# Kernel optimization log

Hardware: AMD Instinct MI355X
Metric: run time of the kernel (lower is better)

## Reference

```python
import jax, jax.numpy as jnp
import numpy as np

N_NODES = 20000


def gcn_layer(x, W, b, src, dst, n):
    # linear transform first (as in PyG GCNConv)
    h = x @ W  # [N, out]
    # add self-loops
    loop = jnp.arange(n, dtype=src.dtype)
    src_f = jnp.concatenate([src, loop])
    dst_f = jnp.concatenate([dst, loop])
    # symmetric degree normalization: deg computed on destination (col) index
    ones = jnp.ones_like(dst_f, dtype=h.dtype)
    deg = jax.ops.segment_sum(ones, dst_f, num_segments=n)
    dinv = jnp.where(deg > 0, jax.lax.rsqrt(deg), 0.0)
    norm = dinv[src_f] * dinv[dst_f]  # [E+N]
    # gather-normalize-scatter aggregation
    msgs = h[src_f] * norm[:, None]  # [E+N, out]
    out = jax.ops.segment_sum(msgs, dst_f, num_segments=n)
    return out + b


def setup_inputs() -> dict:
    key = jax.random.key(0)
    k = jax.random.split(key, 6)
    x = jax.random.normal(k[0], (N_NODES, 256), dtype=jnp.float32)
    edge_index = jax.random.randint(k[1], (2, 320000), 0, N_NODES, dtype=jnp.int64)
    s1 = 1.0 / np.sqrt(256)
    s2 = 1.0 / np.sqrt(1600)
    W1 = jax.random.uniform(k[2], (256, 1600), jnp.float32, -s1, s1)
    b1 = jnp.zeros((1600,), jnp.float32)
    W2 = jax.random.uniform(k[3], (1600, 400), jnp.float32, -s2, s2)
    b2 = jnp.zeros((400,), jnp.float32)
    return {"x": x, "edge_index": edge_index, "W1": W1, "b1": b1, "W2": W2, "b2": b2}


def reference(x, edge_index, W1, b1, W2, b2):
    src, dst = edge_index[0], edge_index[1]
    n = x.shape[0]
    h = jax.nn.relu(gcn_layer(x, W1, b1, src, dst, n))
    return gcn_layer(h, W2, b2, src, dst, n)
```

## Files before the change

### kernel.cpp

```cpp
#include <hip/hip_runtime.h>
#include <hip/hip_bf16.h>
#include <stdint.h>

typedef _Float16 f16;
typedef _Float16 f16x8 __attribute__((ext_vector_type(8)));
typedef _Float16 f16v4 __attribute__((ext_vector_type(4)));
typedef float f32x4 __attribute__((ext_vector_type(4)));

__device__ __forceinline__ void gload_lds16(const f16* g, f16* l) {
  __builtin_amdgcn_global_load_lds(
      (const __attribute__((address_space(1))) void*)g,
      (__attribute__((address_space(3))) void*)l, 16, 0, 0);
}

__device__ __forceinline__ int edge_at(const void* ep, int isI64, long long idx) {
  if (isI64) return (int)((const long long*)ep)[idx];
  return ((const int*)ep)[idx];
}

__global__ void detect_kernel(const unsigned int* __restrict__ e, int* __restrict__ flag) {
  __shared__ int any;
  if (threadIdx.x == 0) any = 0;
  __syncthreads();
  for (int idx = 1 + 2 * (int)threadIdx.x; idx < 4096; idx += 512) {
    if (e[idx] != 0u) any = 1;
  }
  __syncthreads();
  if (threadIdx.x == 0) flag[0] = any ? 0 : 1;
}

__global__ void deg_kernel(const void* __restrict__ ep, const int* __restrict__ flag,
                           int* __restrict__ indeg, int E) {
  int e = blockIdx.x * blockDim.x + threadIdx.x;
  if (e >= E) return;
  int i64 = flag[0];
  int d = edge_at(ep, i64, (long long)E + e);
  atomicAdd(&indeg[d], 1);
}

__global__ void dinv_kernel(const int* __restrict__ indeg, float* __restrict__ dinv, int n) {
  int i = blockIdx.x * blockDim.x + threadIdx.x;
  if (i < n) dinv[i] = rsqrtf((float)(indeg[i] + 1));
}

__global__ __launch_bounds__(1024) void prefix_kernel(const int* __restrict__ indeg,
                                                      int* __restrict__ rowptr, int n) {
  __shared__ int wsum[16];
  int t = threadIdx.x;
  int lane = t & 63;
  int w = t >> 6;
  int carry = 0;
  if (t == 0) rowptr[0] = 0;
  for (int base = 0; base < n; base += 1024) {
    int i = base + t;
    int v = (i < n) ? indeg[i] : 0;
    int sv = v;
#pragma unroll
    for (int off = 1; off < 64; off <<= 1) {
      int u = __shfl_up(sv, off, 64);
      if (lane >= off) sv += u;
    }
    if (lane == 63) wsum[w] = sv;
    __syncthreads();
    if (w == 0 && lane < 16) {
      int ws = wsum[lane];
#pragma unroll
      for (int off = 1; off < 16; off <<= 1) {
        int u = __shfl_up(ws, off, 64);
        if (lane >= off) ws += u;
      }
      wsum[lane] = ws;
    }
    __syncthreads();
    int woff = (w > 0) ? wsum[w - 1] : 0;
    if (i < n) rowptr[i + 1] = carry + woff + sv;
    carry += wsum[15];
    __syncthreads();
  }
}

__global__ void scatter_kernel(const void* __restrict__ ep, const int* __restrict__ flag,
                               const int* __restrict__ rowptr, int* __restrict__ cursor,
                               int* __restrict__ colsrc, int E) {
  int e = blockIdx.x * blockDim.x + threadIdx.x;
  if (e >= E) return;
  int i64 = flag[0];
  int s = edge_at(ep, i64, (long long)e);
  int d = edge_at(ep, i64, (long long)E + e);
  int pos = atomicAdd(&cursor[d], 1);
  colsrc[rowptr[d] + pos] = s;
}

__global__ __launch_bounds__(256) void agg1_kernel(const float* __restrict__ x,
                                                   const float* __restrict__ dinv,
                                                   const int* __restrict__ rowptr,
                                                   const int* __restrict__ colsrc,
                                                   f16* __restrict__ xa, int n) {
  int wave = threadIdx.x >> 6;
  int lane = threadIdx.x & 63;
  int i = blockIdx.x * 4 + wave;
  if (i >= n) return;
  const float4* xp = (const float4*)x;
  float di = dinv[i];
  float4 s = xp[(size_t)i * 64 + lane];
  float ax = di * s.x, ay = di * s.y, az = di * s.z, aw = di * s.w;
  float bx = 0.f, by = 0.f, bz = 0.f, bw = 0.f;
  int beg = rowptr[i], end = rowptr[i + 1];
  int j = beg;
  for (; j + 3 < end; j += 4) {
    int s0 = colsrc[j], s1 = colsrc[j + 1], s2 = colsrc[j + 2], s3 = colsrc[j + 3];
    float w0 = dinv[s0], w1 = dinv[s1], w2 = dinv[s2], w3 = dinv[s3];
    float4 v0 = xp[(size_t)s0 * 64 + lane];
    float4 v1 = xp[(size_t)s1 * 64 + lane];
    float4 v2 = xp[(size_t)s2 * 64 + lane];
    float4 v3 = xp[(size_t)s3 * 64 + lane];
    ax += w0 * v0.x + w2 * v2.x; ay += w0 * v0.y + w2 * v2.y;
    az += w0 * v0.z + w2 * v2.z; aw += w0 * v0.w + w2 * v2.w;
    bx += w1 * v1.x + w3 * v3.x; by += w1 * v1.y + w3 * v3.y;
    bz += w1 * v1.z + w3 * v3.z; bw += w1 * v1.w + w3 * v3.w;
  }
  for (; j < end; ++j) {
    int s0 = colsrc[j];
    float w0 = dinv[s0];
    float4 v0 = xp[(size_t)s0 * 64 + lane];
    ax += w0 * v0.x; ay += w0 * v0.y; az += w0 * v0.z; aw += w0 * v0.w;
  }
  f16v4 r;
  r[0] = (f16)(di * (ax + bx));
  r[1] = (f16)(di * (ay + by));
  r[2] = (f16)(di * (az + bz));
  r[3] = (f16)(di * (aw + bw));
  *(f16v4*)&xa[(size_t)i * 256 + lane * 4] = r;
}

__global__ __launch_bounds__(256) void agg2_kernel(const f16* __restrict__ g,
                                                   const float* __restrict__ dinv,
                                                   const int* __restrict__ rowptr,
                                                   const int* __restrict__ colsrc,
                                                   const float* __restrict__ bias,
                                                   float* __restrict__ out, int n, int F) {
  int wave = threadIdx.x >> 6;
  int lane = threadIdx.x & 63;
  int i = blockIdx.x * 4 + wave;
  if (i >= n) return;
  int base = lane * 8;
  if (base >= F) return;
  float di = dinv[i];
  f16x8 sv = *(const f16x8*)&g[(size_t)i * F + base];
  float a[8], b[8];
#pragma unroll
  for (int r = 0; r < 8; ++r) { a[r] = di * (float)sv[r]; b[r] = 0.f; }
  int beg = rowptr[i], end = rowptr[i + 1];
  int j = beg;
  for (; j + 1 < end; j += 2) {
    int s0 = colsrc[j], s1 = colsrc[j + 1];
    float w0 = dinv[s0], w1 = dinv[s1];
    f16x8 v0 = *(const f16x8*)&g[(size_t)s0 * F + base];
    f16x8 v1 = *(const f16x8*)&g[(size_t)s1 * F + base];
#pragma unroll
    for (int r = 0; r < 8; ++r) { a[r] += w0 * (float)v0[r]; b[r] += w1 * (float)v1[r]; }
  }
  if (j < end) {
    int s0 = colsrc[j];
    float w0 = dinv[s0];
    f16x8 v0 = *(const f16x8*)&g[(size_t)s0 * F + base];
#pragma unroll
    for (int r = 0; r < 8; ++r) a[r] += w0 * (float)v0[r];
  }
  float4 o0, o1;
  float4 bv0 = *(const float4*)&bias[base];
  float4 bv1 = *(const float4*)&bias[base + 4];
  o0.x = di * (a[0] + b[0]) + bv0.x; o0.y = di * (a[1] + b[1]) + bv0.y;
  o0.z = di * (a[2] + b[2]) + bv0.z; o0.w = di * (a[3] + b[3]) + bv0.w;
  o1.x = di * (a[4] + b[4]) + bv1.x; o1.y = di * (a[5] + b[5]) + bv1.y;
  o1.z = di * (a[6] + b[6]) + bv1.z; o1.w = di * (a[7] + b[7]) + bv1.w;
  *(float4*)&out[(size_t)i * F + base] = o0;
  *(float4*)&out[(size_t)i * F + base + 4] = o1;
}

__global__ void castT_kernel(const float* __restrict__ W, f16* __restrict__ Wt, int K, int N) {
  int idx = blockIdx.x * 256 + threadIdx.x;
  if (idx >= K * N) return;
  int k = idx / N;
  int nn = idx - k * N;
  Wt[(size_t)nn * K + k] = (f16)W[idx];
}

__global__ __launch_bounds__(256) void gemm1_f16(
    const f16* __restrict__ A, const f16* __restrict__ B,
    const float* __restrict__ bias, f16* __restrict__ C,
    int M, int N, int K) {
  __shared__ __align__(16) f16 smem[2 * 128 * 64];
  f16* sA = smem;
  f16* sB = smem + 128 * 64;
  const int m0 = blockIdx.y * 128;
  const int n0 = blockIdx.x * 128;
  const int lane = threadIdx.x & 63;
  const int wave = threadIdx.x >> 6;
  const int wm = (wave & 1) * 64;
  const int wn = (wave >> 1) * 64;
  const int lrow = lane & 15;
  const int quad = lane >> 4;

  f32x4 acc[4][4];
#pragma unroll
  for (int i = 0; i < 4; ++i)
#pragma unroll
    for (int j = 0; j < 4; ++j) acc[i][j] = (f32x4)(0.f);

  for (int k0 = 0; k0 < K; k0 += 64) {
#pragma unroll
    for (int i = 0; i < 4; ++i) {
      int ch = (i * 4 + wave) * 64 + lane;
      int r = ch >> 3;
      int cg = (ch & 7) ^ (r & 7);
      int gr = min(m0 + r, M - 1);
      gload_lds16(&A[(size_t)gr * K + k0 + cg * 8], &sA[(size_t)(i * 4 + wave) * 512]);
      int gn = min(n0 + r, N - 1);
      gload_lds16(&B[(size_t)gn * K + k0 + cg * 8], &sB[(size_t)(i * 4 + wave) * 512]);
    }
    __syncthreads();
#pragma unroll
    for (int kk = 0; kk < 2; ++kk) {
      f16x8 af[4], bf[4];
      int cg = quad + kk * 4;
#pragma unroll
      for (int i = 0; i < 4; ++i) {
        int ra = wm + i * 16 + lrow;
        af[i] = *(const f16x8*)&sA[ra * 64 + ((cg ^ (ra & 7)) * 8)];
        int rb = wn + i * 16 + lrow;
        bf[i] = *(const f16x8*)&sB[rb * 64 + ((cg ^ (rb & 7)) * 8)];
      }
#pragma unroll
      for (int i = 0; i < 4; ++i)
#pragma unroll
        for (int j = 0; j < 4; ++j)
          acc[i][j] = __builtin_amdgcn_mfma_f32_16x16x32_f16(af[i], bf[j], acc[i][j], 0, 0, 0);
    }
    __syncthreads();
  }

  const int crow = quad * 4;
  const int ccol = lane & 15;
#pragma unroll
  for (int j = 0; j < 4; ++j) {
    int col = wn + j * 16 + ccol;
    int gcol = n0 + col;
    float bv = (gcol < N) ? bias[gcol] : 0.f;
#pragma unroll
    for (int i = 0; i < 4; ++i) {
#pragma unroll
      for (int r = 0; r < 4; ++r) {
        int row = wm + i * 16 + crow + r;
        smem[row * 128 + col] = (f16)fmaxf(acc[i][j][r] + bv, 0.f);
      }
    }
  }
  __syncthreads();
#pragma unroll
  for (int i = 0; i < 8; ++i) {
    int ch = i * 256 + (int)threadIdx.x;
    int r = ch >> 4;
    int cc = ch & 15;
    int grow = m0 + r;
    int gcol = n0 + cc * 8;
    if (grow < M && gcol < N)
      *(uint4*)&C[(size_t)grow * N + gcol] = *(const uint4*)&smem[r * 128 + cc * 8];
  }
}

__global__ __launch_bounds__(256) void gemm2_f16(
    const f16* __restrict__ A, const f16* __restrict__ B, f16* __restrict__ C,
    int M, int N, int K) {
  __shared__ __align__(16) f16 smem[128 * 64 + 80 * 64];
  f16* sA = smem;
  f16* sB = smem + 128 * 64;

  const int mtc = (M + 127) >> 7;
  const int ntc = (N + 79) / 80;
  const int fullm = mtc & ~7;
  const int full = fullm * ntc;
  int idf = blockIdx.x;
  int mt, nt;
  if (idf < full) {
    int gsz = 8 * ntc;
    int grp = idf / gsz;
    int r = idf - grp * gsz;
    mt = grp * 8 + (r & 7);
    nt = r >> 3;
  } else {
    int r = idf - full;
    int rem = mtc - fullm;
    mt = fullm + r % rem;
    nt = r / rem;
  }
  const int m0 = mt * 128;
  const int n0 = nt * 80;
  const int lane = threadIdx.x & 63;
  const int wave = threadIdx.x >> 6;
  const int wm = wave * 32;
  const int lrow = lane & 15;
  const int quad = lane >> 4;

  f32x4 acc[2][5];
#pragma unroll
  for (int i = 0; i < 2; ++i)
#pragma unroll
    for (int j = 0; j < 5; ++j) acc[i][j] = (f32x4)(0.f);

  for (int k0 = 0; k0 < K; k0 += 64) {
#pragma unroll
    for (int i = 0; i < 4; ++i) {
      int ch = (i * 4 + wave) * 64 + lane;
      int r = ch >> 3;
      int cg = (ch & 7) ^ (r & 7);
      int gr = min(m0 + r, M - 1);
      gload_lds16(&A[(size_t)gr * K + k0 + cg * 8], &sA[(size_t)(i * 4 + wave) * 512]);
    }
#pragma unroll
    for (int i = 0; i < 3; ++i) {
      if (i * 4 + wave < 10) {
        int ch = (i * 4 + wave) * 64 + lane;
        int r = ch >> 3;
        int cg = (ch & 7) ^ (r & 7);
        gload_lds16(&B[(size_t)(n0 + r) * K + k0 + cg * 8], &sB[(size_t)(i * 4 + wave) * 512]);
      }
    }
    __syncthreads();
#pragma unroll
    for (int kk = 0; kk < 2; ++kk) {
      f16x8 af[2], bf[5];
      int cg = quad + kk * 4;
#pragma unroll
      for (int i = 0; i < 2; ++i) {
        int ra = wm + i * 16 + lrow;
        af[i] = *(const f16x8*)&sA[ra * 64 + ((cg ^ (ra & 7)) * 8)];
      }
#pragma unroll
      for (int j = 0; j < 5; ++j) {
        int rb = j * 16 + lrow;
        bf[j] = *(const f16x8*)&sB[rb * 64 + ((cg ^ (rb & 7)) * 8)];
      }
#pragma unroll
      for (int i = 0; i < 2; ++i)
#pragma unroll
        for (int j = 0; j < 5; ++j)
          acc[i][j] = __builtin_amdgcn_mfma_f32_16x16x32_f16(af[i], bf[j], acc[i][j], 0, 0, 0);
    }
    __syncthreads();
  }

  const int crow = quad * 4;
  const int ccol = lane & 15;
#pragma unroll
  for (int j = 0; j < 5; ++j) {
    int col = j * 16 + ccol;
#pragma unroll
    for (int i = 0; i < 2; ++i) {
#pragma unroll
      for (int r = 0; r < 4; ++r) {
        int row = wm + i * 16 + crow + r;
        smem[row * 80 + col] = (f16)acc[i][j][r];
      }
    }
  }
  __syncthreads();
#pragma unroll
  for (int i = 0; i < 5; ++i) {
    int ch = i * 256 + (int)threadIdx.x;
    int r = ch / 10;
    int rem = ch - 10 * r;
    int grow = m0 + r;
    if (grow < M)
      *(uint4*)&C[(size_t)grow * N + n0 + rem * 8] = *(const uint4*)&smem[r * 80 + rem * 8];
  }
}

extern "C" void kernel_launch(void* const* d_in, const int* in_sizes, int n_in,
                              void* d_out, int out_size, void* d_ws, size_t ws_size,
                              hipStream_t stream) {
  const float* x = (const float*)d_in[0];
  const void* edges = d_in[1];
  const float* W1 = (const float*)d_in[2];
  const float* b1 = (const float*)d_in[3];
  const float* W2 = (const float*)d_in[4];
  const float* b2 = (const float*)d_in[5];
  float* out = (float*)d_out;

  const int N1 = in_sizes[3];
  const int N2 = in_sizes[5];
  const int K1 = in_sizes[2] / N1;
  const int K2 = in_sizes[4] / N2;
  const int n = in_sizes[0] / K1;
  const int E = in_sizes[1] / 2;

  char* ws = (char*)d_ws;
  size_t o = 0;
  auto take = [&](size_t bytes) {
    char* p = ws + o;
    o += (bytes + 255) & ~(size_t)255;
    return p;
  };
  int* indeg = (int*)take((size_t)n * 4);
  int* cursor = (int*)take((size_t)n * 4);
  int* flag = (int*)take(4);
  size_t zero_bytes = o;
  int* rowptr = (int*)take((size_t)(n + 1) * 4);
  int* colsrc = (int*)take((size_t)E * 4);
  float* dinv = (float*)take((size_t)n * 4);
  f16* xa = (f16*)take((size_t)n * K1 * 2);
  f16* w1t = (f16*)take((size_t)K1 * N1 * 2);
  f16* w2t = (f16*)take((size_t)K2 * N2 * 2);
  f16* h = (f16*)take((size_t)n * N1 * 2);
  f16* g = (f16*)take((size_t)n * N2 * 2);

  hipMemsetAsync(d_ws, 0, zero_bytes, stream);

  detect_kernel<<<1, 256, 0, stream>>>((const unsigned int*)edges, flag);
  deg_kernel<<<(E + 255) / 256, 256, 0, stream>>>(edges, flag, indeg, E);
  dinv_kernel<<<(n + 255) / 256, 256, 0, stream>>>(indeg, dinv, n);
  prefix_kernel<<<1, 1024, 0, stream>>>(indeg, rowptr, n);
  scatter_kernel<<<(E + 255) / 256, 256, 0, stream>>>(edges, flag, rowptr, cursor, colsrc, E);

  castT_kernel<<<(K1 * N1 + 255) / 256, 256, 0, stream>>>(W1, w1t, K1, N1);
  castT_kernel<<<(K2 * N2 + 255) / 256, 256, 0, stream>>>(W2, w2t, K2, N2);

  agg1_kernel<<<(n + 3) / 4, 256, 0, stream>>>(x, dinv, rowptr, colsrc, xa, n);
  {
    dim3 grid((N1 + 127) / 128, (n + 127) / 128);
    gemm1_f16<<<grid, 256, 0, stream>>>(xa, w1t, b1, h, n, N1, K1);
  }
  {
    int mtc = (n + 127) / 128;
    int ntc = (N2 + 79) / 80;
    gemm2_f16<<<mtc * ntc, 256, 0, stream>>>(h, w2t, g, n, N2, K2);
  }
  agg2_kernel<<<(n + 3) / 4, 256, 0, stream>>>(g, dinv, rowptr, colsrc, b2, out, n, N2);
}
```

Baseline: 302.5 us.

## Pre-scale features by source dinv and drop per-edge dinv gathers

Folds the source-side degree normalization into the features before aggregation. Layer 1 now runs an xcast kernel that writes x*dinv as fp16, and gemm2 scales its output rows by dinv, so both aggregation loops skip the per-edge dinv gather and multiply. The change also merges the dinv computation into the prefix kernel, merges the two weight-cast launches, and widens the agg2 unroll to four edges. Gather traffic in agg1 is halved by reading fp16 instead of fp32, at the cost of an extra cast pass and buffer plus earlier fp16 rounding of the scaled inputs.

```diff
diff --git a/kernel.cpp b/kernel.cpp
--- a/kernel.cpp
+++ b/kernel.cpp
@@ -38,13 +38,9 @@
   atomicAdd(&indeg[d], 1);
 }
 
-__global__ void dinv_kernel(const int* __restrict__ indeg, float* __restrict__ dinv, int n) {
-  int i = blockIdx.x * blockDim.x + threadIdx.x;
-  if (i < n) dinv[i] = rsqrtf((float)(indeg[i] + 1));
-}
-
 __global__ __launch_bounds__(1024) void prefix_kernel(const int* __restrict__ indeg,
-                                                      int* __restrict__ rowptr, int n) {
+                                                      int* __restrict__ rowptr,
+                                                      float* __restrict__ dinv, int n) {
   __shared__ int wsum[16];
   int t = threadIdx.x;
   int lane = t & 63;
@@ -54,6 +50,7 @@
   for (int base = 0; base < n; base += 1024) {
     int i = base + t;
     int v = (i < n) ? indeg[i] : 0;
+    if (i < n) dinv[i] = rsqrtf((float)(v + 1));
     int sv = v;
 #pragma unroll
     for (int off = 1; off < 64; off <<= 1) {
@@ -91,7 +88,22 @@
   colsrc[rowptr[d] + pos] = s;
 }
 
-__global__ __launch_bounds__(256) void agg1_kernel(const float* __restrict__ x,
+__global__ void xcast_kernel(const float* __restrict__ x, const float* __restrict__ dinv,
+                             f16* __restrict__ xs, int n) {
+  int c = blockIdx.x * 256 + threadIdx.x;
+  if (c >= n * 64) return;
+  int row = c >> 6;
+  float d = dinv[row];
+  float4 v = ((const float4*)x)[c];
+  f16v4 r;
+  r[0] = (f16)(d * v.x);
+  r[1] = (f16)(d * v.y);
+  r[2] = (f16)(d * v.z);
+  r[3] = (f16)(d * v.w);
+  ((f16v4*)xs)[c] = r;
+}
+
+__global__ __launch_bounds__(256) void agg1_kernel(const f16* __restrict__ xs,
                                                    const float* __restrict__ dinv,
                                                    const int* __restrict__ rowptr,
                                                    const int* __restrict__ colsrc,
@@ -100,40 +112,38 @@
   int lane = threadIdx.x & 63;
   int i = blockIdx.x * 4 + wave;
   if (i >= n) return;
-  const float4* xp = (const float4*)x;
+  const f16v4* xp = (const f16v4*)xs;
   float di = dinv[i];
-  float4 s = xp[(size_t)i * 64 + lane];
-  float ax = di * s.x, ay = di * s.y, az = di * s.z, aw = di * s.w;
-  float bx = 0.f, by = 0.f, bz = 0.f, bw = 0.f;
+  f16v4 s = xp[(size_t)i * 64 + lane];
+  float a0 = (float)s[0], a1 = (float)s[1], a2 = (float)s[2], a3 = (float)s[3];
+  float b0 = 0.f, b1 = 0.f, b2 = 0.f, b3 = 0.f;
   int beg = rowptr[i], end = rowptr[i + 1];
   int j = beg;
   for (; j + 3 < end; j += 4) {
     int s0 = colsrc[j], s1 = colsrc[j + 1], s2 = colsrc[j + 2], s3 = colsrc[j + 3];
-    float w0 = dinv[s0], w1 = dinv[s1], w2 = dinv[s2], w3 = dinv[s3];
-    float4 v0 = xp[(size_t)s0 * 64 + lane];
-    float4 v1 = xp[(size_t)s1 * 64 + lane];
-    float4 v2 = xp[(size_t)s2 * 64 + lane];
-    float4 v3 = xp[(size_t)s3 * 64 + lane];
-    ax += w0 * v0.x + w2 * v2.x; ay += w0 * v0.y + w2 * v2.y;
-    az += w0 * v0.z + w2 * v2.z; aw += w0 * v0.w + w2 * v2.w;
-    bx += w1 * v1.x + w3 * v3.x; by += w1 * v1.y + w3 * v3.y;
-    bz += w1 * v1.z + w3 * v3.z; bw += w1 * v1.w + w3 * v3.w;
+    f16v4 v0 = xp[(size_t)s0 * 64 + lane];
+    f16v4 v1 = xp[(size_t)s1 * 64 + lane];
+    f16v4 v2 = xp[(size_t)s2 * 64 + lane];
+    f16v4 v3 = xp[(size_t)s3 * 64 + lane];
+    a0 += (float)v0[0] + (float)v2[0]; a1 += (float)v0[1] + (float)v2[1];
+    a2 += (float)v0[2] + (float)v2[2]; a3 += (float)v0[3] + (float)v2[3];
+    b0 += (float)v1[0] + (float)v3[0]; b1 += (float)v1[1] + (float)v3[1];
+    b2 += (float)v1[2] + (float)v3[2]; b3 += (float)v1[3] + (float)v3[3];
   }
   for (; j < end; ++j) {
     int s0 = colsrc[j];
-    float w0 = dinv[s0];
-    float4 v0 = xp[(size_t)s0 * 64 + lane];
-    ax += w0 * v0.x; ay += w0 * v0.y; az += w0 * v0.z; aw += w0 * v0.w;
+    f16v4 v0 = xp[(size_t)s0 * 64 + lane];
+    a0 += (float)v0[0]; a1 += (float)v0[1]; a2 += (float)v0[2]; a3 += (float)v0[3];
   }
   f16v4 r;
-  r[0] = (f16)(di * (ax + bx));
-  r[1] = (f16)(di * (ay + by));
-  r[2] = (f16)(di * (az + bz));
-  r[3] = (f16)(di * (aw + bw));
+  r[0] = (f16)(di * (a0 + b0));
+  r[1] = (f16)(di * (a1 + b1));
+  r[2] = (f16)(di * (a2 + b2));
+  r[3] = (f16)(di * (a3 + b3));
   *(f16v4*)&xa[(size_t)i * 256 + lane * 4] = r;
 }
 
-__global__ __launch_bounds__(256) void agg2_kernel(const f16* __restrict__ g,
+__global__ __launch_bounds__(256) void agg2_kernel(const f16* __restrict__ gs,
                                                    const float* __restrict__ dinv,
                                                    const int* __restrict__ rowptr,
                                                    const int* __restrict__ colsrc,
@@ -146,26 +156,29 @@
   int base = lane * 8;
   if (base >= F) return;
   float di = dinv[i];
-  f16x8 sv = *(const f16x8*)&g[(size_t)i * F + base];
+  f16x8 sv = *(const f16x8*)&gs[(size_t)i * F + base];
   float a[8], b[8];
 #pragma unroll
-  for (int r = 0; r < 8; ++r) { a[r] = di * (float)sv[r]; b[r] = 0.f; }
+  for (int r = 0; r < 8; ++r) { a[r] = (float)sv[r]; b[r] = 0.f; }
   int beg = rowptr[i], end = rowptr[i + 1];
   int j = beg;
-  for (; j + 1 < end; j += 2) {
-    int s0 = colsrc[j], s1 = colsrc[j + 1];
-    float w0 = dinv[s0], w1 = dinv[s1];
-    f16x8 v0 = *(const f16x8*)&g[(size_t)s0 * F + base];
-    f16x8 v1 = *(const f16x8*)&g[(size_t)s1 * F + base];
-#pragma unroll
-    for (int r = 0; r < 8; ++r) { a[r] += w0 * (float)v0[r]; b[r] += w1 * (float)v1[r]; }
-  }
-  if (j < end) {
+  for (; j + 3 < end; j += 4) {
+    int s0 = colsrc[j], s1 = colsrc[j + 1], s2 = colsrc[j + 2], s3 = colsrc[j + 3];
+    f16x8 v0 = *(const f16x8*)&gs[(size_t)s0 * F + base];
+    f16x8 v1 = *(const f16x8*)&gs[(size_t)s1 * F + base];
+    f16x8 v2 = *(const f16x8*)&gs[(size_t)s2 * F + base];
+    f16x8 v3 = *(const f16x8*)&gs[(size_t)s3 * F + base];
+#pragma unroll
+    for (int r = 0; r < 8; ++r) {
+      a[r] += (float)v0[r] + (float)v2[r];
+      b[r] += (float)v1[r] + (float)v3[r];
+    }
+  }
+  for (; j < end; ++j) {
     int s0 = colsrc[j];
-    float w0 = dinv[s0];
-    f16x8 v0 = *(const f16x8*)&g[(size_t)s0 * F + base];
-#pragma unroll
-    for (int r = 0; r < 8; ++r) a[r] += w0 * (float)v0[r];
+    f16x8 v0 = *(const f16x8*)&gs[(size_t)s0 * F + base];
+#pragma unroll
+    for (int r = 0; r < 8; ++r) a[r] += (float)v0[r];
   }
   float4 o0, o1;
   float4 bv0 = *(const float4*)&bias[base];
@@ -178,12 +191,22 @@
   *(float4*)&out[(size_t)i * F + base + 4] = o1;
 }
 
-__global__ void castT_kernel(const float* __restrict__ W, f16* __restrict__ Wt, int K, int N) {
+__global__ void castT_kernel(const float* __restrict__ W1, f16* __restrict__ W1t, int K1, int N1,
+                             const float* __restrict__ W2, f16* __restrict__ W2t, int K2, int N2) {
   int idx = blockIdx.x * 256 + threadIdx.x;
-  if (idx >= K * N) return;
-  int k = idx / N;
-  int nn = idx - k * N;
-  Wt[(size_t)nn * K + k] = (f16)W[idx];
+  int t1 = K1 * N1;
+  if (idx < t1) {
+    int k = idx / N1;
+    int nn = idx - k * N1;
+    W1t[(size_t)nn * K1 + k] = (f16)W1[idx];
+  } else {
+    idx -= t1;
+    if (idx < K2 * N2) {
+      int k = idx / N2;
+      int nn = idx - k * N2;
+      W2t[(size_t)nn * K2 + k] = (f16)W2[idx];
+    }
+  }
 }
 
 __global__ __launch_bounds__(256) void gemm1_f16(
@@ -270,7 +293,8 @@
 }
 
 __global__ __launch_bounds__(256) void gemm2_f16(
-    const f16* __restrict__ A, const f16* __restrict__ B, f16* __restrict__ C,
+    const f16* __restrict__ A, const f16* __restrict__ B,
+    const float* __restrict__ dinv, f16* __restrict__ C,
     int M, int N, int K) {
   __shared__ __align__(16) f16 smem[128 * 64 + 80 * 64];
   f16* sA = smem;
@@ -352,6 +376,14 @@
 
   const int crow = quad * 4;
   const int ccol = lane & 15;
+  float dsc[2][4];
+#pragma unroll
+  for (int i = 0; i < 2; ++i)
+#pragma unroll
+    for (int r = 0; r < 4; ++r) {
+      int grow = m0 + wm + i * 16 + crow + r;
+      dsc[i][r] = dinv[min(grow, M - 1)];
+    }
 #pragma unroll
   for (int j = 0; j < 5; ++j) {
     int col = j * 16 + ccol;
@@ -360,7 +392,7 @@
 #pragma unroll
       for (int r = 0; r < 4; ++r) {
         int row = wm + i * 16 + crow + r;
-        smem[row * 80 + col] = (f16)acc[i][j][r];
+        smem[row * 80 + col] = (f16)(acc[i][j][r] * dsc[i][r]);
       }
     }
   }
@@ -408,6 +440,7 @@
   int* rowptr = (int*)take((size_t)(n + 1) * 4);
   int* colsrc = (int*)take((size_t)E * 4);
   float* dinv = (float*)take((size_t)n * 4);
+  f16* xs = (f16*)take((size_t)n * K1 * 2);
   f16* xa = (f16*)take((size_t)n * K1 * 2);
   f16* w1t = (f16*)take((size_t)K1 * N1 * 2);
   f16* w2t = (f16*)take((size_t)K2 * N2 * 2);
@@ -418,14 +451,14 @@
 
   detect_kernel<<<1, 256, 0, stream>>>((const unsigned int*)edges, flag);
   deg_kernel<<<(E + 255) / 256, 256, 0, stream>>>(edges, flag, indeg, E);
-  dinv_kernel<<<(n + 255) / 256, 256, 0, stream>>>(indeg, dinv, n);
-  prefix_kernel<<<1, 1024, 0, stream>>>(indeg, rowptr, n);
+  prefix_kernel<<<1, 1024, 0, stream>>>(indeg, rowptr, dinv, n);
   scatter_kernel<<<(E + 255) / 256, 256, 0, stream>>>(edges, flag, rowptr, cursor, colsrc, E);
 
-  castT_kernel<<<(K1 * N1 + 255) / 256, 256, 0, stream>>>(W1, w1t, K1, N1);
-  castT_kernel<<<(K2 * N2 + 255) / 256, 256, 0, stream>>>(W2, w2t, K2, N2);
-
-  agg1_kernel<<<(n + 3) / 4, 256, 0, stream>>>(x, dinv, rowptr, colsrc, xa, n);
+  castT_kernel<<<(K1 * N1 + K2 * N2 + 255) / 256, 256, 0, stream>>>(W1, w1t, K1, N1, W2, w2t,
+                                                                    K2, N2);
+  xcast_kernel<<<(n * 64 + 255) / 256, 256, 0, stream>>>(x, dinv, xs, n);
+
+  agg1_kernel<<<(n + 3) / 4, 256, 0, stream>>>(xs, dinv, rowptr, colsrc, xa, n);
   {
     dim3 grid((N1 + 127) / 128, (n + 127) / 128);
     gemm1_f16<<<grid, 256, 0, stream>>>(xa, w1t, b1, h, n, N1, K1);
@@ -433,7 +466,7 @@
   {
     int mtc = (n + 127) / 128;
     int ntc = (N2 + 79) / 80;
-    gemm2_f16<<<mtc * ntc, 256, 0, stream>>>(h, w2t, g, n, N2, K2);
+    gemm2_f16<<<mtc * ntc, 256, 0, stream>>>(h, w2t, dinv, g, n, N2, K2);
   }
   agg2_kernel<<<(n + 3) / 4, 256, 0, stream>>>(g, dinv, rowptr, colsrc, b2, out, n, N2);
 }
```

New measurement: 291.9 us. 1.04x faster.
